# Kernel tuning notes

Measured on AMD Instinct MI355X. Metric: run time of the kernel, lower is better.

Reference implementation:

```python
import math
import jax, jax.numpy as jnp
import numpy as np

B, S, E, H = 4, 2048, 1024, 16
D = E // H


def setup_inputs() -> dict:
    key = jax.random.key(0)
    k1, k2, k3 = jax.random.split(key, 3)
    return {
        "hidden_state": jax.random.normal(k1, (B, S, E), dtype=jnp.float32),
        "attention_mask": jnp.zeros((B, 1, 1, S), dtype=jnp.float32),
        "W_attn": jax.random.normal(k2, (E, 3 * E), dtype=jnp.float32) * 0.02,
        "b_attn": jnp.zeros((3 * E,), dtype=jnp.float32),
        "W_proj": jax.random.normal(k3, (E, E), dtype=jnp.float32) * 0.02,
        "b_proj": jnp.zeros((E,), dtype=jnp.float32),
    }


def reference(hidden_state, attention_mask, W_attn, b_attn, W_proj, b_proj):
    b, s, e = hidden_state.shape
    d = e // H
    # c_attn (HF Conv1D): x @ W + b -> [B,S,3E]
    x = hidden_state @ W_attn + b_attn
    q, k, v = jnp.split(x, 3, axis=-1)
    # split heads -> [B,H,S,D]
    q = q.reshape(b, s, H, d).transpose(0, 2, 1, 3)
    k = k.reshape(b, s, H, d).transpose(0, 2, 1, 3)
    v = v.reshape(b, s, H, d).transpose(0, 2, 1, 3)
    # scores [B,H,S,S]; scale=True divides by sqrt(d_head)
    w = jnp.einsum("bhqd,bhkd->bhqk", q, k) / math.sqrt(d)
    causal = jnp.tril(jnp.ones((s, s), dtype=w.dtype))[None, None]
    w = w * causal + (-10000.0) * (1.0 - causal)
    w = w + attention_mask
    w = jax.nn.softmax(w, axis=-1)  # attn_dropout p=0 (eval)
    out = jnp.einsum("bhqk,bhkd->bhqd", w, v)
    # merge heads -> [B,S,E]
    out = out.transpose(0, 2, 1, 3).reshape(b, s, e)
    # c_proj; resid_dropout p=0 (eval)
    return out @ W_proj + b_proj
```

## Files before the change

### kernel.cpp

```cpp
#include <hip/hip_runtime.h>
#include <hip/hip_bf16.h>

typedef __attribute__((ext_vector_type(4))) float f32x4;
typedef __attribute__((ext_vector_type(8))) short bf16x8;

#define B_SZ  4
#define S_LEN 2048
#define EMB   1024
#define NH    16
#define DH    64
#define E3    3072
#define QKLD  2048
#define LOG2E 1.4426950408889634f
#define SC2   (0.125f * LOG2E)
#define MSTAT 14.0f

#define VMCNT(N) asm volatile("s_waitcnt vmcnt(" #N ")" ::: "memory")
#define RAWBAR() asm volatile("s_barrier" ::: "memory")

__device__ __forceinline__ void gload_lds16(const void* g, void* l) {
  __builtin_amdgcn_global_load_lds((const __attribute__((address_space(1))) void*)g,
                                   (__attribute__((address_space(3))) void*)l, 16, 0, 0);
}

__device__ __forceinline__ float bf2f(unsigned short u) {
  union { unsigned int i; float f; } c;
  c.i = (unsigned int)u << 16;
  return c.f;
}

__device__ __forceinline__ unsigned pack_bf16_rtz(float hi, float lo) {
  union { float f; unsigned u; } a, b;
  a.f = hi; b.f = lo;
  return (a.u & 0xffff0000u) | (b.u >> 16);
}

__global__ void cvt_bf16_kernel(const float* __restrict__ in,
                                __hip_bfloat16* __restrict__ out, int n) {
  const int i = (blockIdx.x * 256 + threadIdx.x) * 4;
  if (i >= n) return;
  const float4 v = *(const float4*)(in + i);
  __align__(8) __hip_bfloat16 o[4];
  o[0] = __float2bfloat16(v.x); o[1] = __float2bfloat16(v.y);
  o[2] = __float2bfloat16(v.z); o[3] = __float2bfloat16(v.w);
  *(uint2*)(out + i) = *(const uint2*)o;
}

__global__ __launch_bounds__(256)
void transpose_cvt(const float* __restrict__ in, __hip_bfloat16* __restrict__ out,
                   int R, int C) {
  __shared__ float tile[32][33];
  const int tx = threadIdx.x & 31, ty = threadIdx.x >> 5;
  const int c = blockIdx.x * 32 + tx;
#pragma unroll
  for (int i = 0; i < 32; i += 8)
    tile[ty + i][tx] = in[(size_t)(blockIdx.y * 32 + ty + i) * C + c];
  __syncthreads();
  const int r2 = blockIdx.y * 32 + tx;
#pragma unroll
  for (int i = 0; i < 32; i += 8)
    out[(size_t)(blockIdx.x * 32 + ty + i) * R + r2] = __float2bfloat16(tile[tx][ty + i]);
}

template <int EPI>
__global__ __launch_bounds__(512, 2)
void gemm_v3(const __hip_bfloat16* __restrict__ A, const __hip_bfloat16* __restrict__ BT,
             const float* __restrict__ bias, void* __restrict__ Cout,
             __hip_bfloat16* __restrict__ vt) {
  __shared__ __attribute__((aligned(16))) char lds[98304];
  const int tid = threadIdx.x;
  const int lane = tid & 63, w = tid >> 6;
  const int lr = lane & 15, lg = lane >> 4, lg4 = lg * 4;
  const int wm = w >> 2, wn = w & 3;
  const int m0 = blockIdx.x * 256, n0 = blockIdx.y * 256;

  const int srow = tid >> 2;
  const int scol = ((tid & 3) ^ ((tid >> 3) & 3)) << 3;
  const __hip_bfloat16* pA = A + (size_t)(m0 + srow) * 1024 + scol;
  const __hip_bfloat16* pB = BT + (size_t)(n0 + srow) * 1024 + scol;
  char* const ldsd = lds + tid * 16;

  const int sw = (lg ^ ((lr >> 1) & 3)) << 4;
  const int abyte = (wm * 128 + lr) * 64 + sw;
  const int bbyte = 16384 + (wn * 64 + lr) * 64 + sw;

  f32x4 acc[8][4] = {};

  gload_lds16(pA,                 ldsd);
  gload_lds16(pA + 131072,        ldsd + 8192);
  gload_lds16(pB,                 ldsd + 16384);
  gload_lds16(pB + 131072,        ldsd + 24576);
  gload_lds16(pA + 32,            ldsd + 32768);
  gload_lds16(pA + 131072 + 32,   ldsd + 32768 + 8192);
  gload_lds16(pB + 32,            ldsd + 32768 + 16384);
  gload_lds16(pB + 131072 + 32,   ldsd + 32768 + 24576);

  int cur = 0;
#pragma unroll 1
  for (int t = 0; t < 32; ++t) {
    if (t < 31) { VMCNT(4); } else { VMCNT(0); }
    RAWBAR();
    if (t + 2 < 32) {
      const int nb = (cur >= 1) ? cur - 1 : 2;
      char* d = ldsd + nb * 32768;
      const __hip_bfloat16* sa = pA + (t + 2) * 32;
      const __hip_bfloat16* sb = pB + (t + 2) * 32;
      gload_lds16(sa,          d);
      gload_lds16(sa + 131072, d + 8192);
      gload_lds16(sb,          d + 16384);
      gload_lds16(sb + 131072, d + 24576);
    }
    const char* base = lds + cur * 32768;
    bf16x8 a[8], b[4];
#pragma unroll
    for (int m = 0; m < 8; ++m) a[m] = *(const bf16x8*)(base + abyte + m * 1024);
#pragma unroll
    for (int n = 0; n < 4; ++n) b[n] = *(const bf16x8*)(base + bbyte + n * 1024);
#pragma unroll
    for (int m = 0; m < 8; ++m)
#pragma unroll
      for (int n = 0; n < 4; ++n)
        acc[m][n] = __builtin_amdgcn_mfma_f32_16x16x32_bf16(a[m], b[n], acc[m][n], 0, 0, 0);
    cur = (cur == 2) ? 0 : cur + 1;
  }

  if (EPI == 0 && n0 >= 2 * EMB) {
#pragma unroll
    for (int m8 = 0; m8 < 8; ++m8) {
      const int rowg0 = m0 + wm * 128 + m8 * 16 + lg4;
      const int bz = rowg0 >> 11, sloc = rowg0 & (S_LEN - 1);
#pragma unroll
      for (int n4 = 0; n4 < 4; ++n4) {
        const int col = n0 + wn * 64 + n4 * 16 + lr;
        const int c2 = col - 2 * EMB;
        const int hh = c2 >> 6, dd = c2 & 63;
        const float bv = bias[col];
        __align__(8) __hip_bfloat16 pb[4];
#pragma unroll
        for (int r = 0; r < 4; ++r) pb[r] = __float2bfloat16(acc[m8][n4][r] + bv);
        *(uint2*)&vt[(size_t)((bz * NH + hh) * DH + dd) * S_LEN + sloc] = *(const uint2*)pb;
      }
    }
  } else if (EPI == 0) {
#pragma unroll
    for (int m8 = 0; m8 < 8; ++m8) {
#pragma unroll
      for (int n4 = 0; n4 < 4; ++n4) {
        const int col = n0 + wn * 64 + n4 * 16 + lr;
        const float bv = bias[col];
#pragma unroll
        for (int r = 0; r < 4; ++r) {
          const int rowg = m0 + wm * 128 + m8 * 16 + lg4 + r;
          ((__hip_bfloat16*)Cout)[(size_t)rowg * QKLD + col] = __float2bfloat16(acc[m8][n4][r] + bv);
        }
      }
    }
  } else {
#pragma unroll
    for (int m8 = 0; m8 < 8; ++m8) {
#pragma unroll
      for (int n4 = 0; n4 < 4; ++n4) {
        const int col = n0 + wn * 64 + n4 * 16 + lr;
        const float bv = bias[col];
#pragma unroll
        for (int r = 0; r < 4; ++r) {
          const int rowg = m0 + wm * 128 + m8 * 16 + lg4 + r;
          ((float*)Cout)[(size_t)rowg * EMB + col] = acc[m8][n4][r] + bv;
        }
      }
    }
  }
}

template <bool DIAG>
__device__ __forceinline__ void qstep(const char* Ks, const char* Vs,
                                      __hip_bfloat16 (*Psw)[72], const __hip_bfloat16* Msb,
                                      int msoff, const bf16x8 (&aq)[2], f32x4 (&acc)[4],
                                      float& lrun, int lr, int lg, int lg4, int wq) {
  f32x4 sacc[4] = {};
  __builtin_amdgcn_s_setprio(1);
#pragma unroll
  for (int kt = 0; kt < 4; ++kt)
#pragma unroll
    for (int ks = 0; ks < 2; ++ks) {
      const bf16x8 kb = *(const bf16x8*)(Ks + (kt * 16 + lr) * 128 +
                                         (((ks * 4 + lg) ^ (lr & 7)) << 4));
      sacc[kt] = __builtin_amdgcn_mfma_f32_16x16x32_bf16(kb, aq[ks], sacc[kt], 0, 0, 0);
    }
  __builtin_amdgcn_s_setprio(0);
#pragma unroll
  for (int kt = 0; kt < 4; ++kt) {
    const ushort4 mb = *(const ushort4*)&Msb[msoff + kt * 16 + lg4];
    float pp[4];
#pragma unroll
    for (int r = 0; r < 4; ++r) {
      float sv = sacc[kt][r] * SC2 + bf2f(((const unsigned short*)&mb)[r]);
      if (DIAG && (kt * 16 + lg4 + r > wq)) sv = -1.0e9f;
      pp[r] = __builtin_amdgcn_exp2f(sv);
    }
    lrun += (pp[0] + pp[1]) + (pp[2] + pp[3]);
    uint2 uu;
    uu.x = pack_bf16_rtz(pp[1], pp[0]);
    uu.y = pack_bf16_rtz(pp[3], pp[2]);
    *(uint2*)&Psw[lr][kt * 16 + lg4] = uu;
  }
#pragma unroll
  for (int ks = 0; ks < 2; ++ks) {
    const bf16x8 pa = *(const bf16x8*)&Psw[lr][ks * 32 + lg * 8];
    __builtin_amdgcn_s_setprio(1);
#pragma unroll
    for (int dt = 0; dt < 4; ++dt) {
      const bf16x8 vb = *(const bf16x8*)(Vs + (dt * 16 + lr) * 128 +
                                         (((ks * 4 + lg) ^ (lr & 7)) << 4));
      acc[dt] = __builtin_amdgcn_mfma_f32_16x16x32_bf16(pa, vb, acc[dt], 0, 0, 0);
    }
    __builtin_amdgcn_s_setprio(0);
  }
}

template <bool DIAGA>
__device__ __forceinline__ void qstep2(const char* Ks, const char* Vs,
                                       __hip_bfloat16 (*PsA)[72], __hip_bfloat16 (*PsB)[72],
                                       const __hip_bfloat16* Msb, int msoff,
                                       const bf16x8 (&aqA)[2], const bf16x8 (&aqB)[2],
                                       f32x4 (&accA)[4], f32x4 (&accB)[4],
                                       float& lA, float& lB, int lr, int lg, int lg4, int wq) {
  f32x4 sA[4] = {}, sB[4] = {};
  __builtin_amdgcn_s_setprio(1);
#pragma unroll
  for (int kt = 0; kt < 4; ++kt)
#pragma unroll
    for (int ks = 0; ks < 2; ++ks) {
      const bf16x8 kb = *(const bf16x8*)(Ks + (kt * 16 + lr) * 128 +
                                         (((ks * 4 + lg) ^ (lr & 7)) << 4));
      sA[kt] = __builtin_amdgcn_mfma_f32_16x16x32_bf16(kb, aqA[ks], sA[kt], 0, 0, 0);
      sB[kt] = __builtin_amdgcn_mfma_f32_16x16x32_bf16(kb, aqB[ks], sB[kt], 0, 0, 0);
    }
  __builtin_amdgcn_s_setprio(0);
#pragma unroll
  for (int kt = 0; kt < 4; ++kt) {
    const ushort4 mb = *(const ushort4*)&Msb[msoff + kt * 16 + lg4];
    float pA[4], pB[4];
#pragma unroll
    for (int r = 0; r < 4; ++r) {
      const float mkr = bf2f(((const unsigned short*)&mb)[r]);
      float svA = sA[kt][r] * SC2 + mkr;
      if (DIAGA && (kt * 16 + lg4 + r > wq)) svA = -1.0e9f;
      const float svB = sB[kt][r] * SC2 + mkr;
      pA[r] = __builtin_amdgcn_exp2f(svA);
      pB[r] = __builtin_amdgcn_exp2f(svB);
    }
    lA += (pA[0] + pA[1]) + (pA[2] + pA[3]);
    lB += (pB[0] + pB[1]) + (pB[2] + pB[3]);
    uint2 ua, ub;
    ua.x = pack_bf16_rtz(pA[1], pA[0]);
    ua.y = pack_bf16_rtz(pA[3], pA[2]);
    ub.x = pack_bf16_rtz(pB[1], pB[0]);
    ub.y = pack_bf16_rtz(pB[3], pB[2]);
    *(uint2*)&PsA[lr][kt * 16 + lg4] = ua;
    *(uint2*)&PsB[lr][kt * 16 + lg4] = ub;
  }
#pragma unroll
  for (int ks = 0; ks < 2; ++ks) {
    const bf16x8 paA = *(const bf16x8*)&PsA[lr][ks * 32 + lg * 8];
    const bf16x8 paB = *(const bf16x8*)&PsB[lr][ks * 32 + lg * 8];
    __builtin_amdgcn_s_setprio(1);
#pragma unroll
    for (int dt = 0; dt < 4; ++dt) {
      const bf16x8 vb = *(const bf16x8*)(Vs + (dt * 16 + lr) * 128 +
                                         (((ks * 4 + lg) ^ (lr & 7)) << 4));
      accA[dt] = __builtin_amdgcn_mfma_f32_16x16x32_bf16(paA, vb, accA[dt], 0, 0, 0);
      accB[dt] = __builtin_amdgcn_mfma_f32_16x16x32_bf16(paB, vb, accB[dt], 0, 0, 0);
    }
    __builtin_amdgcn_s_setprio(0);
  }
}

#define STAGE_LOAD_BUMP()                                                          \
  {                                                                                \
    kpre[0] = *(const bf16x8*)kcur;                                                \
    kpre[1] = *(const bf16x8*)(kcur + 8 * QKLD);                                   \
    vpre[0] = *(const bf16x8*)vcur;                                                \
    vpre[1] = *(const bf16x8*)(vcur + 8 * S_LEN);                                  \
    kcur += 64 * QKLD;                                                             \
    vcur += 64;                                                                    \
  }

#define TILE_SYNC(PREFETCH)                                                        \
  {                                                                                \
    __syncthreads();                                                               \
    *(bf16x8*)kw0 = kpre[0];                                                       \
    *(bf16x8*)(kw0 + 1024) = kpre[1];                                              \
    *(bf16x8*)vw0 = vpre[0];                                                       \
    *(bf16x8*)(vw0 + 1024) = vpre[1];                                              \
    __syncthreads();                                                               \
    if (PREFETCH) STAGE_LOAD_BUMP();                                               \
  }

__global__ __launch_bounds__(256, 4)
void flash_attn10(const __hip_bfloat16* __restrict__ qk, const __hip_bfloat16* __restrict__ vt,
                  const float* __restrict__ amask, __hip_bfloat16* __restrict__ aout) {
  const int j = blockIdx.x;
  const int g = (j & 7) + 8 * (j >> 7);
  const int x = (((j >> 3) & 15) + (((j >> 8) & 3) << 2)) & 15;
  const int h = g >> 2, bz = g & 3;

  const int tid = threadIdx.x;
  const int lane = tid & 63, w = tid >> 6;
  const int lr = lane & 15, lg = lane >> 4, lg4 = lg * 4;
  const int wq = w * 16 + lr;

  const int qta = x, qtb = 31 - x;

  __shared__ __align__(16) __hip_bfloat16 Ks[64 * 64];
  __shared__ __align__(16) __hip_bfloat16 Vs[64 * 64];
  __shared__ __align__(16) __hip_bfloat16 Ps[4][2][16][72];
  __shared__ __align__(8)  __hip_bfloat16 Msb[S_LEN];

  {
    const int e = tid * 8;
    const f32x4 m0v = *(const f32x4*)&amask[bz * S_LEN + e];
    const f32x4 m1v = *(const f32x4*)&amask[bz * S_LEN + e + 4];
    __align__(16) __hip_bfloat16 mb[8];
#pragma unroll
    for (int jj = 0; jj < 4; ++jj) {
      mb[jj]     = __float2bfloat16(m0v[jj] * LOG2E - MSTAT);
      mb[jj + 4] = __float2bfloat16(m1v[jj] * LOG2E - MSTAT);
    }
    *(uint4*)&Msb[e] = *(const uint4*)mb;
  }

  bf16x8 aqA[2], aqB[2];
  {
    const __hip_bfloat16* qpA =
        qk + (size_t)(bz * S_LEN + qta * 64 + w * 16 + lr) * QKLD + h * DH + lg * 8;
    aqA[0] = *(const bf16x8*)qpA; aqA[1] = *(const bf16x8*)(qpA + 32);
    const __hip_bfloat16* qpB =
        qk + (size_t)(bz * S_LEN + qtb * 64 + w * 16 + lr) * QKLD + h * DH + lg * 8;
    aqB[0] = *(const bf16x8*)qpB; aqB[1] = *(const bf16x8*)(qpB + 32);
  }

  f32x4 accA[4] = {}, accB[4] = {};
  float lA = 0.f, lB = 0.f;

  const __hip_bfloat16* kcur = qk + (size_t)bz * S_LEN * QKLD + EMB + h * DH +
                               (size_t)(w * 16 + (lane >> 3)) * QKLD + (lane & 7) * 8;
  const __hip_bfloat16* vcur = vt + (size_t)((bz * NH + h) * DH + w * 16 + (lane >> 3)) * S_LEN +
                               (lane & 7) * 8;
  char* kw0 = (char*)Ks + (w * 16 + (lane >> 3)) * 128 + (((lane & 7) ^ (lane >> 3)) << 4);
  char* vw0 = (char*)Vs + (w * 16 + (lane >> 3)) * 128 + (((lane & 7) ^ (lane >> 3)) << 4);

  bf16x8 kpre[2], vpre[2];
  STAGE_LOAD_BUMP();

  int msoff = 0;
  for (int t = 0; t < qta; ++t) {
    TILE_SYNC(true);
    qstep2<false>((char*)Ks, (char*)Vs, Ps[w][0], Ps[w][1], Msb, msoff,
                  aqA, aqB, accA, accB, lA, lB, lr, lg, lg4, wq);
    msoff += 64;
  }
  TILE_SYNC(true);
  qstep2<true>((char*)Ks, (char*)Vs, Ps[w][0], Ps[w][1], Msb, msoff,
               aqA, aqB, accA, accB, lA, lB, lr, lg, lg4, wq);
  msoff += 64;
  for (int t = qta + 1; t < qtb; ++t) {
    TILE_SYNC(true);
    qstep<false>((char*)Ks, (char*)Vs, Ps[w][1], Msb, msoff, aqB, accB, lB, lr, lg, lg4, wq);
    msoff += 64;
  }
  TILE_SYNC(false);
  qstep<true>((char*)Ks, (char*)Vs, Ps[w][1], Msb, msoff, aqB, accB, lB, lr, lg, lg4, wq);

  lA += __shfl_xor(lA, 16); lA += __shfl_xor(lA, 32);
  lB += __shfl_xor(lB, 16); lB += __shfl_xor(lB, 32);
  float lqA[4], lqB[4];
#pragma unroll
  for (int r = 0; r < 4; ++r) {
    lqA[r] = __shfl(lA, lg4 + r);
    lqB[r] = __shfl(lB, lg4 + r);
  }
#pragma unroll
  for (int dt = 0; dt < 4; ++dt)
#pragma unroll
    for (int r = 0; r < 4; ++r) {
      const int qA = qta * 64 + w * 16 + lg4 + r;
      aout[(size_t)(bz * S_LEN + qA) * EMB + h * DH + dt * 16 + lr] =
          __float2bfloat16(accA[dt][r] / lqA[r]);
      const int qB = qtb * 64 + w * 16 + lg4 + r;
      aout[(size_t)(bz * S_LEN + qB) * EMB + h * DH + dt * 16 + lr] =
          __float2bfloat16(accB[dt][r] / lqB[r]);
    }
}

extern "C" void kernel_launch(void* const* d_in, const int* in_sizes, int n_in,
                              void* d_out, int out_size, void* d_ws, size_t ws_size,
                              hipStream_t stream) {
  const float* hidden = (const float*)d_in[0];
  const float* amask  = (const float*)d_in[1];
  const float* W_attn = (const float*)d_in[2];
  const float* b_attn = (const float*)d_in[3];
  const float* W_proj = (const float*)d_in[4];
  const float* b_proj = (const float*)d_in[5];
  float* out = (float*)d_out;

  char* ws = (char*)d_ws;
  __hip_bfloat16* hbf   = (__hip_bfloat16*)(ws);
  __hip_bfloat16* WaT   = (__hip_bfloat16*)(ws + 16777216);
  __hip_bfloat16* WpT   = (__hip_bfloat16*)(ws + 23068672);
  __hip_bfloat16* qkQK  = (__hip_bfloat16*)(ws + 25165824);
  __hip_bfloat16* vt    = (__hip_bfloat16*)(ws + 58720256);
  __hip_bfloat16* aoutb = (__hip_bfloat16*)(ws + 75497472);

  cvt_bf16_kernel<<<dim3(8192), dim3(256), 0, stream>>>(hidden, hbf, B_SZ * S_LEN * EMB);
  transpose_cvt<<<dim3(96, 32), dim3(256), 0, stream>>>(W_attn, WaT, EMB, E3);
  transpose_cvt<<<dim3(32, 32), dim3(256), 0, stream>>>(W_proj, WpT, EMB, EMB);
  gemm_v3<0><<<dim3(32, 12), dim3(512), 0, stream>>>(hbf, WaT, b_attn, qkQK, vt);
  flash_attn10<<<dim3(1024), dim3(256), 0, stream>>>(qkQK, vt, amask, aoutb);
  gemm_v3<1><<<dim3(32, 4), dim3(512), 0, stream>>>(aoutb, WpT, b_proj, out, nullptr);
}
```

Before: 183.9 us.

## Shrink GEMM tile to 128x256 with 4 waves and XCD-aware block remap

```diff
diff --git a/kernel.cpp b/kernel.cpp
--- a/kernel.cpp
+++ b/kernel.cpp
@@ -63,113 +63,127 @@
 }
 
 template <int EPI>
-__global__ __launch_bounds__(512, 2)
-void gemm_v3(const __hip_bfloat16* __restrict__ A, const __hip_bfloat16* __restrict__ BT,
+__global__ __launch_bounds__(256, 2)
+void gemm_v4(const __hip_bfloat16* __restrict__ A, const __hip_bfloat16* __restrict__ BT,
              const float* __restrict__ bias, void* __restrict__ Cout,
              __hip_bfloat16* __restrict__ vt) {
-  __shared__ __attribute__((aligned(16))) char lds[98304];
+  __shared__ __attribute__((aligned(16))) char lds[73728];
   const int tid = threadIdx.x;
   const int lane = tid & 63, w = tid >> 6;
   const int lr = lane & 15, lg = lane >> 4, lg4 = lg * 4;
-  const int wm = w >> 2, wn = w & 3;
-  const int m0 = blockIdx.x * 256, n0 = blockIdx.y * 256;
-
-  const int srow = tid >> 2;
-  const int scol = ((tid & 3) ^ ((tid >> 3) & 3)) << 3;
-  const __hip_bfloat16* pA = A + (size_t)(m0 + srow) * 1024 + scol;
-  const __hip_bfloat16* pB = BT + (size_t)(n0 + srow) * 1024 + scol;
-  char* const ldsd = lds + tid * 16;
+  const int wm = w >> 1, wn = w & 1;
+
+  const int j = blockIdx.x;
+  const int g = (j & 7) * ((int)gridDim.x >> 3) + (j >> 3);
+  const int bx = g & 63, by = g >> 6;
+  const int m0 = bx * 128, n0 = by * 256;
+
+  const int ar1 = tid >> 2;
+  const int ar2 = ar1 + 64;
+  const int cg = tid & 3;
+  const int ac1 = (cg ^ ((ar1 >> 1) & 3)) * 8;
+  const int ac2 = (cg ^ ((ar2 >> 1) & 3)) * 8;
+  const __hip_bfloat16* pa1 = A + (size_t)(m0 + ar1) * 1024 + ac1;
+  const __hip_bfloat16* pa2 = A + (size_t)(m0 + ar2) * 1024 + ac2;
+  const int br0 = tid >> 2, br1 = br0 + 64, br2 = br0 + 128, br3 = br0 + 192;
+  const __hip_bfloat16* pb0 = BT + (size_t)(n0 + br0) * 1024 + (cg ^ ((br0 >> 1) & 3)) * 8;
+  const __hip_bfloat16* pb1 = BT + (size_t)(n0 + br1) * 1024 + (cg ^ ((br1 >> 1) & 3)) * 8;
+  const __hip_bfloat16* pb2 = BT + (size_t)(n0 + br2) * 1024 + (cg ^ ((br2 >> 1) & 3)) * 8;
+  const __hip_bfloat16* pb3 = BT + (size_t)(n0 + br3) * 1024 + (cg ^ ((br3 >> 1) & 3)) * 8;
+  char* const dA1 = lds + tid * 16;
+  char* const dA2 = lds + 4096 + tid * 16;
+  char* const dB0 = lds + 8192 + tid * 16;
+  char* const dB1 = lds + 8192 + 4096 + tid * 16;
+  char* const dB2 = lds + 8192 + 8192 + tid * 16;
+  char* const dB3 = lds + 8192 + 12288 + tid * 16;
+
+#define STG_V4(BUF, T) { \
+    const int off_ = (T) * 32; \
+    gload_lds16(pa1 + off_, dA1 + (BUF) * 24576); \
+    gload_lds16(pa2 + off_, dA2 + (BUF) * 24576); \
+    gload_lds16(pb0 + off_, dB0 + (BUF) * 24576); \
+    gload_lds16(pb1 + off_, dB1 + (BUF) * 24576); \
+    gload_lds16(pb2 + off_, dB2 + (BUF) * 24576); \
+    gload_lds16(pb3 + off_, dB3 + (BUF) * 24576); }
 
   const int sw = (lg ^ ((lr >> 1) & 3)) << 4;
-  const int abyte = (wm * 128 + lr) * 64 + sw;
-  const int bbyte = 16384 + (wn * 64 + lr) * 64 + sw;
-
-  f32x4 acc[8][4] = {};
-
-  gload_lds16(pA,                 ldsd);
-  gload_lds16(pA + 131072,        ldsd + 8192);
-  gload_lds16(pB,                 ldsd + 16384);
-  gload_lds16(pB + 131072,        ldsd + 24576);
-  gload_lds16(pA + 32,            ldsd + 32768);
-  gload_lds16(pA + 131072 + 32,   ldsd + 32768 + 8192);
-  gload_lds16(pB + 32,            ldsd + 32768 + 16384);
-  gload_lds16(pB + 131072 + 32,   ldsd + 32768 + 24576);
+  const int abyte = (wm * 64 + lr) * 64 + sw;
+  const int bbyte = 8192 + (wn * 128 + lr) * 64 + sw;
+
+  f32x4 acc[4][8] = {};
+
+  STG_V4(0, 0); STG_V4(1, 1);
 
   int cur = 0;
 #pragma unroll 1
   for (int t = 0; t < 32; ++t) {
-    if (t < 31) { VMCNT(4); } else { VMCNT(0); }
+    if (t < 31) { VMCNT(6); } else { VMCNT(0); }
     RAWBAR();
     if (t + 2 < 32) {
       const int nb = (cur >= 1) ? cur - 1 : 2;
-      char* d = ldsd + nb * 32768;
-      const __hip_bfloat16* sa = pA + (t + 2) * 32;
-      const __hip_bfloat16* sb = pB + (t + 2) * 32;
-      gload_lds16(sa,          d);
-      gload_lds16(sa + 131072, d + 8192);
-      gload_lds16(sb,          d + 16384);
-      gload_lds16(sb + 131072, d + 24576);
-    }
-    const char* base = lds + cur * 32768;
-    bf16x8 a[8], b[4];
-#pragma unroll
-    for (int m = 0; m < 8; ++m) a[m] = *(const bf16x8*)(base + abyte + m * 1024);
-#pragma unroll
-    for (int n = 0; n < 4; ++n) b[n] = *(const bf16x8*)(base + bbyte + n * 1024);
-#pragma unroll
-    for (int m = 0; m < 8; ++m)
-#pragma unroll
-      for (int n = 0; n < 4; ++n)
+      STG_V4(nb, t + 2);
+    }
+    const char* base = lds + cur * 24576;
+    bf16x8 a[4], b[8];
+#pragma unroll
+    for (int m = 0; m < 4; ++m) a[m] = *(const bf16x8*)(base + abyte + m * 1024);
+#pragma unroll
+    for (int n = 0; n < 8; ++n) b[n] = *(const bf16x8*)(base + bbyte + n * 1024);
+#pragma unroll
+    for (int m = 0; m < 4; ++m)
+#pragma unroll
+      for (int n = 0; n < 8; ++n)
         acc[m][n] = __builtin_amdgcn_mfma_f32_16x16x32_bf16(a[m], b[n], acc[m][n], 0, 0, 0);
     cur = (cur == 2) ? 0 : cur + 1;
   }
 
   if (EPI == 0 && n0 >= 2 * EMB) {
 #pragma unroll
-    for (int m8 = 0; m8 < 8; ++m8) {
-      const int rowg0 = m0 + wm * 128 + m8 * 16 + lg4;
+    for (int m = 0; m < 4; ++m) {
+      const int rowg0 = m0 + wm * 64 + m * 16 + lg4;
       const int bz = rowg0 >> 11, sloc = rowg0 & (S_LEN - 1);
 #pragma unroll
-      for (int n4 = 0; n4 < 4; ++n4) {
-        const int col = n0 + wn * 64 + n4 * 16 + lr;
+      for (int n = 0; n < 8; ++n) {
+        const int col = n0 + wn * 128 + n * 16 + lr;
         const int c2 = col - 2 * EMB;
         const int hh = c2 >> 6, dd = c2 & 63;
         const float bv = bias[col];
         __align__(8) __hip_bfloat16 pb[4];
 #pragma unroll
-        for (int r = 0; r < 4; ++r) pb[r] = __float2bfloat16(acc[m8][n4][r] + bv);
+        for (int r = 0; r < 4; ++r) pb[r] = __float2bfloat16(acc[m][n][r] + bv);
         *(uint2*)&vt[(size_t)((bz * NH + hh) * DH + dd) * S_LEN + sloc] = *(const uint2*)pb;
       }
     }
   } else if (EPI == 0) {
 #pragma unroll
-    for (int m8 = 0; m8 < 8; ++m8) {
-#pragma unroll
-      for (int n4 = 0; n4 < 4; ++n4) {
-        const int col = n0 + wn * 64 + n4 * 16 + lr;
+    for (int m = 0; m < 4; ++m) {
+#pragma unroll
+      for (int n = 0; n < 8; ++n) {
+        const int col = n0 + wn * 128 + n * 16 + lr;
         const float bv = bias[col];
 #pragma unroll
         for (int r = 0; r < 4; ++r) {
-          const int rowg = m0 + wm * 128 + m8 * 16 + lg4 + r;
-          ((__hip_bfloat16*)Cout)[(size_t)rowg * QKLD + col] = __float2bfloat16(acc[m8][n4][r] + bv);
+          const int rowg = m0 + wm * 64 + m * 16 + lg4 + r;
+          ((__hip_bfloat16*)Cout)[(size_t)rowg * QKLD + col] = __float2bfloat16(acc[m][n][r] + bv);
         }
       }
     }
   } else {
 #pragma unroll
-    for (int m8 = 0; m8 < 8; ++m8) {
-#pragma unroll
-      for (int n4 = 0; n4 < 4; ++n4) {
-        const int col = n0 + wn * 64 + n4 * 16 + lr;
+    for (int m = 0; m < 4; ++m) {
+#pragma unroll
+      for (int n = 0; n < 8; ++n) {
+        const int col = n0 + wn * 128 + n * 16 + lr;
         const float bv = bias[col];
 #pragma unroll
         for (int r = 0; r < 4; ++r) {
-          const int rowg = m0 + wm * 128 + m8 * 16 + lg4 + r;
-          ((float*)Cout)[(size_t)rowg * EMB + col] = acc[m8][n4][r] + bv;
+          const int rowg = m0 + wm * 64 + m * 16 + lg4 + r;
+          ((float*)Cout)[(size_t)rowg * EMB + col] = acc[m][n][r] + bv;
         }
       }
     }
   }
+#undef STG_V4
 }
 
 template <bool DIAG>
@@ -415,7 +429,7 @@
   cvt_bf16_kernel<<<dim3(8192), dim3(256), 0, stream>>>(hidden, hbf, B_SZ * S_LEN * EMB);
   transpose_cvt<<<dim3(96, 32), dim3(256), 0, stream>>>(W_attn, WaT, EMB, E3);
   transpose_cvt<<<dim3(32, 32), dim3(256), 0, stream>>>(W_proj, WpT, EMB, EMB);
-  gemm_v3<0><<<dim3(32, 12), dim3(512), 0, stream>>>(hbf, WaT, b_attn, qkQK, vt);
+  gemm_v4<0><<<dim3(768), dim3(256), 0, stream>>>(hbf, WaT, b_attn, qkQK, vt);
   flash_attn10<<<dim3(1024), dim3(256), 0, stream>>>(qkQK, vt, amask, aoutb);
-  gemm_v3<1><<<dim3(32, 4), dim3(512), 0, stream>>>(aoutb, WpT, b_proj, out, nullptr);
-}
+  gemm_v4<1><<<dim3(256), dim3(256), 0, stream>>>(aoutb, WpT, b_proj, out, nullptr);
+}
```

Result: faster. 172.8 us (-6.0%).
